# Kernel tuning notes

Measured on AMD Instinct MI355X. Metric: run time of the kernel, lower is better.

Reference implementation:

```python
import jax, jax.numpy as jnp
import numpy as np

N_COARSE, N_FINE, N_EDGE, W, DEPTH = 16384, 65536, 393216, 128, 2


def _mlp_params(key, fan_in, width, out):
    k1, k2 = jax.random.split(key)
    w1 = jax.random.normal(k1, (fan_in, width), jnp.float32) / np.sqrt(fan_in)
    b1 = jnp.zeros((width,), jnp.float32)
    w2 = jax.random.normal(k2, (width, out), jnp.float32) / np.sqrt(width)
    b2 = jnp.zeros((out,), jnp.float32)
    return w1, b1, w2, b2


def setup_inputs() -> dict:
    key = jax.random.key(0)
    ks = jax.random.split(key, 16)
    v = jax.random.normal(ks[0], (N_COARSE, W), jnp.float32)
    c_skip = jax.random.normal(ks[1], (N_FINE, W), jnp.float32)
    e_skip = jax.random.normal(ks[2], (N_EDGE, W), jnp.float32)
    edge_index_skip = jax.random.randint(ks[3], (2, N_EDGE), 0, N_FINE, jnp.int32)
    batch_skip = jnp.zeros((N_FINE,), jnp.int32)  # single graph
    cluster = jax.random.randint(ks[4], (N_FINE,), 0, N_COARSE, jnp.int32)
    rel_pos = jax.random.normal(ks[5], (N_FINE, 1), jnp.float32)  # scalar rel pos (scalar_rel_pos=True)

    # unpooling FNN: (W + 1) -> W -> W
    uw1, ub1, uw2, ub2 = _mlp_params(ks[6], W + 1, W, W)
    # InteractionNetwork MLPs, stacked over DEPTH layers
    ew1 = []; eb1 = []; ew2 = []; eb2 = []
    nw1 = []; nb1 = []; nw2 = []; nb2 = []
    for i in range(DEPTH):
        a, b, c, d = _mlp_params(ks[7 + i], 3 * W, W, W)  # edge MLP: [e, v_s, v_r]
        ew1.append(a); eb1.append(b); ew2.append(c); eb2.append(d)
        a, b, c, d = _mlp_params(ks[9 + i], 2 * W, W, W)  # node MLP: [v, aggr(e)]
        nw1.append(a); nb1.append(b); nw2.append(c); nb2.append(d)
    stk = lambda xs: jnp.stack(xs, 0)
    return {
        'v': v, 'c_skip': c_skip, 'e_skip': e_skip, 'rel_pos': rel_pos,
        'unpool_w1': uw1, 'unpool_b1': ub1, 'unpool_w2': uw2, 'unpool_b2': ub2,
        'edge_w1': stk(ew1), 'edge_b1': stk(eb1), 'edge_w2': stk(ew2), 'edge_b2': stk(eb2),
        'node_w1': stk(nw1), 'node_b1': stk(nb1), 'node_w2': stk(nw2), 'node_b2': stk(nb2),
        'edge_index_skip': edge_index_skip, 'cluster': cluster, 'batch_skip': batch_skip,
    }


def _mlp(x, w1, b1, w2, b2):
    return jax.nn.selu(x @ w1 + b1) @ w2 + b2


def reference(v, c_skip, e_skip, rel_pos,
              unpool_w1, unpool_b1, unpool_w2, unpool_b2,
              edge_w1, edge_b1, edge_w2, edge_b2,
              node_w1, node_b1, node_w2, node_b2,
              edge_index_skip, cluster, batch_skip):
    # --- MeshUpMP: gather coarse features to fine nodes, mix with rel. pos. ---
    h = jnp.concatenate([v[cluster], rel_pos], axis=-1)            # [N_fine, W+1]
    v = _mlp(h, unpool_w1, unpool_b1, unpool_w2, unpool_b2)        # [N_fine, W]
    v = v + c_skip
    e = e_skip
    s, r = edge_index_skip[0], edge_index_skip[1]
    n_nodes = v.shape[0]
    # --- stacked InteractionNetwork layers (residual edge+node updates) ---
    for i in range(edge_w1.shape[0]):
        msg = jnp.concatenate([e, v[s], v[r]], axis=-1)            # [E, 3W]
        e = e + _mlp(msg, edge_w1[i], edge_b1[i], edge_w2[i], edge_b2[i])
        agg = jax.ops.segment_sum(e, r, num_segments=n_nodes)      # sum aggregation
        nin = jnp.concatenate([v, agg], axis=-1)                   # [N, 2W]
        v = v + _mlp(nin, node_w1[i], node_b1[i], node_w2[i], node_b2[i])
    return v
```

## Files before the change

kernel.cpp:

```cpp
#include <hip/hip_runtime.h>
#include <hip/hip_bf16.h>
#include <stdint.h>

#define NCOARSE 16384
#define NFINE   65536
#define NEDGE   393216

typedef __bf16 bf16;
typedef bf16 bf16x8 __attribute__((ext_vector_type(8)));
typedef bf16 bf16x4 __attribute__((ext_vector_type(4)));
typedef float f32x4 __attribute__((ext_vector_type(4)));

__device__ __forceinline__ float selu_f(float x) {
    return x > 0.f ? 1.0507009873554805f * x
                   : 1.7580993408473766f * (__expf(x) - 1.f);
}

__device__ __forceinline__ bf16x8 cvt8(f32x4 lo, f32x4 hi) {
    bf16x8 r;
    r[0] = (bf16)lo[0]; r[1] = (bf16)lo[1]; r[2] = (bf16)lo[2]; r[3] = (bf16)lo[3];
    r[4] = (bf16)hi[0]; r[5] = (bf16)hi[1]; r[6] = (bf16)hi[2]; r[7] = (bf16)hi[3];
    return r;
}

__global__ void prep_weights(const float* __restrict__ uw1, const float* __restrict__ uw2,
                             const float* __restrict__ ew1, const float* __restrict__ ew2,
                             const float* __restrict__ nw1, const float* __restrict__ nw2,
                             bf16* __restrict__ wb)
{
    int i = blockIdx.x * 256 + threadIdx.x;
    float v;
    if (i < 16384) {
        int j = i; int k = (j >> 12) * 32 + (j & 31), n = (j & 4095) >> 5;
        v = uw1[k * 128 + n];
    } else if (i < 32768) {
        int j = i - 16384; int k = (j >> 12) * 32 + (j & 31), n = (j & 4095) >> 5;
        v = uw2[k * 128 + n];
    } else if (i < 131072) {
        int j = i - 32768; int l = j / 49152; j -= l * 49152;
        int k = (j >> 12) * 32 + (j & 31), n = (j & 4095) >> 5;
        v = ew1[l * 49152 + k * 128 + n];
    } else if (i < 163840) {
        int j = i - 131072; int l = j >> 14; j &= 16383;
        int k = (j >> 12) * 32 + (j & 31), n = (j & 4095) >> 5;
        v = ew2[l * 16384 + k * 128 + n];
    } else if (i < 229376) {
        int j = i - 163840; int l = j >> 15; j &= 32767;
        int k = (j >> 12) * 32 + (j & 31), n = (j & 4095) >> 5;
        v = nw1[l * 32768 + k * 128 + n];
    } else {
        int j = i - 229376; int l = j >> 14; j &= 16383;
        int k = (j >> 12) * 32 + (j & 31), n = (j & 4095) >> 5;
        v = nw2[l * 16384 + k * 128 + n];
    }
    wb[i] = (bf16)v;
}

__global__ void hist_kernel(const int* __restrict__ ei, int* __restrict__ cnt) {
    int e = blockIdx.x * 256 + threadIdx.x;
    if (e < NEDGE) atomicAdd(&cnt[ei[NEDGE + e]], 1);
}

__global__ __launch_bounds__(1024)
void scan_kernel(const int* __restrict__ cnt, int* __restrict__ rowptr,
                 int* __restrict__ cursor) {
    __shared__ int part[1024];
    const int t = threadIdx.x;
    const int base = t * 64;
    int s = 0;
    for (int i = 0; i < 64; ++i) s += cnt[base + i];
    part[t] = s;
    __syncthreads();
    for (int off = 1; off < 1024; off <<= 1) {
        int v = (t >= off) ? part[t - off] : 0;
        __syncthreads();
        part[t] += v;
        __syncthreads();
    }
    int run = part[t] - s;
    for (int i = 0; i < 64; ++i) {
        int c = cnt[base + i];
        rowptr[base + i] = run;
        cursor[base + i] = run;
        run += c;
    }
    if (t == 1023) rowptr[65536] = run;
}

__global__ void scatter_kernel(const int* __restrict__ ei, int* __restrict__ cursor,
                               int* __restrict__ perm) {
    int e = blockIdx.x * 256 + threadIdx.x;
    if (e < NEDGE) {
        int r = ei[NEDGE + e];
        int p = atomicAdd(&cursor[r], 1);
        perm[p] = e;
    }
}

__global__ __launch_bounds__(256)
void agg_kernel(const bf16* __restrict__ e, const int* __restrict__ rowptr,
                const int* __restrict__ perm, bf16* __restrict__ agg) {
    int t = blockIdx.x * 256 + threadIdx.x;
    int node = t >> 3, c0 = (t & 7) * 16;
    int s = rowptr[node], en = rowptr[node + 1];
    float acc[16];
    #pragma unroll
    for (int k = 0; k < 16; ++k) acc[k] = 0.f;
    for (int j = s; j < en; ++j) {
        size_t ed = (size_t)perm[j];
        bf16x8 x0 = *(const bf16x8*)(e + ed * 128 + c0);
        bf16x8 x1 = *(const bf16x8*)(e + ed * 128 + c0 + 8);
        #pragma unroll
        for (int k = 0; k < 8; ++k) { acc[k] += (float)x0[k]; acc[8 + k] += (float)x1[k]; }
    }
    bf16x8 o0, o1;
    #pragma unroll
    for (int k = 0; k < 8; ++k) { o0[k] = (bf16)acc[k]; o1[k] = (bf16)acc[8 + k]; }
    *(bf16x8*)(agg + (size_t)node * 128 + c0) = o0;
    *(bf16x8*)(agg + (size_t)node * 128 + c0 + 8) = o1;
}


#define STAGE_LOAD(wp, st0, st1) do { \
    st0 = *(const bf16x8*)((wp) + tid * 8); \
    st1 = *(const bf16x8*)((wp) + 2048 + tid * 8); } while (0)
#define STAGE_WRITE(buf, st0, st1) do { \
    *(bf16x8*)&(buf)[tid >> 2][(tid & 3) * 8] = st0; \
    *(bf16x8*)&(buf)[(tid + 256) >> 2][(tid & 3) * 8] = st1; } while (0)

template<bool EF32>
__global__ __launch_bounds__(256, 2)
void edge_kernel(const void* __restrict__ e_in_v,
                 bf16* __restrict__ e_out,
                 const bf16* __restrict__ v_bf,
                 const int* __restrict__ ei,
                 const bf16* __restrict__ w1s,
                 const float* __restrict__ b1,
                 const bf16* __restrict__ w2s,
                 const float* __restrict__ b2)
{
    const int tid = threadIdx.x;
    const int wv = tid >> 6, lane = tid & 63;
    const int lr = lane & 15, g = lane >> 4;
    const int wbase = blockIdx.x * 128 + wv * 32;

    __shared__ bf16 wl[2][128][40];
    __shared__ bf16 hid_all[4][32][136];
    bf16 (*hid)[136] = hid_all[wv];

    const float* e_f32 = (const float*)e_in_v;
    const bf16*  e_b16 = (const bf16*)e_in_v;

    int row[2], sidx[2], ridx[2];
    #pragma unroll
    for (int mt = 0; mt < 2; ++mt) {
        row[mt] = wbase + mt * 16 + lr;
        sidx[mt] = ei[row[mt]];
        ridx[mt] = ei[NEDGE + row[mt]];
    }

    bf16x8 be[4][2], bs[4][2], br[4][2];
    #pragma unroll
    for (int ks = 0; ks < 4; ++ks)
        #pragma unroll
        for (int mt = 0; mt < 2; ++mt)
            bs[ks][mt] = *(const bf16x8*)(v_bf + (size_t)sidx[mt] * 128 + ks * 32 + g * 8);
    #pragma unroll
    for (int ks = 0; ks < 4; ++ks)
        #pragma unroll
        for (int mt = 0; mt < 2; ++mt)
            br[ks][mt] = *(const bf16x8*)(v_bf + (size_t)ridx[mt] * 128 + ks * 32 + g * 8);
    if (EF32) {
        f32x4 tlo[4][2], thi[4][2];
        #pragma unroll
        for (int ks = 0; ks < 4; ++ks)
            #pragma unroll
            for (int mt = 0; mt < 2; ++mt) {
                const float* p = e_f32 + (size_t)row[mt] * 128 + ks * 32 + g * 8;
                tlo[ks][mt] = *(const f32x4*)p;
                thi[ks][mt] = *(const f32x4*)(p + 4);
            }
        #pragma unroll
        for (int ks = 0; ks < 4; ++ks)
            #pragma unroll
            for (int mt = 0; mt < 2; ++mt)
                be[ks][mt] = cvt8(tlo[ks][mt], thi[ks][mt]);
    } else {
        #pragma unroll
        for (int ks = 0; ks < 4; ++ks)
            #pragma unroll
            for (int mt = 0; mt < 2; ++mt)
                be[ks][mt] = *(const bf16x8*)(e_b16 + (size_t)row[mt] * 128 + ks * 32 + g * 8);
    }

    bf16x8 st0, st1;
    STAGE_LOAD(w1s, st0, st1);
    STAGE_WRITE(wl[0], st0, st1);
    __syncthreads();

    f32x4 acc1[8][2], acc2[8][2];
    #pragma unroll
    for (int oc = 0; oc < 8; ++oc) {
        f32x4 z = {0.f, 0.f, 0.f, 0.f};
        acc1[oc][0] = z; acc1[oc][1] = z;
    }

    f32x4  eof[8][2];
    bf16x4 eob[8][2];

    #pragma unroll
    for (int s = 0; s < 16; ++s) {
        const int cur = s & 1;
        if (s < 15) {
            const bf16* wp = (s + 1 < 12) ? w1s + (size_t)(s + 1) * 4096
                                          : w2s + (size_t)(s + 1 - 12) * 4096;
            STAGE_LOAD(wp, st0, st1);
        }
        if (s == 12) {
            #pragma unroll
            for (int mt = 0; mt < 2; ++mt)
                #pragma unroll
                for (int oc = 0; oc < 8; ++oc) {
                    const int col = oc * 16 + g * 4;
                    if (EF32) eof[oc][mt] = *(const f32x4*)(e_f32 + (size_t)row[mt] * 128 + col);
                    else      eob[oc][mt] = *(const bf16x4*)(e_b16 + (size_t)row[mt] * 128 + col);
                }
        }
        bf16x8 a[8];
        #pragma unroll
        for (int oc = 0; oc < 8; ++oc)
            a[oc] = *(const bf16x8*)&wl[cur][oc * 16 + lr][g * 8];

        if (s < 12) {
            bf16x8 b0 = (s < 4) ? be[s][0] : (s < 8) ? bs[s - 4][0] : br[s - 8][0];
            bf16x8 b1f = (s < 4) ? be[s][1] : (s < 8) ? bs[s - 4][1] : br[s - 8][1];
            #pragma unroll
            for (int oc = 0; oc < 8; ++oc) {
                acc1[oc][0] = __builtin_amdgcn_mfma_f32_16x16x32_bf16(a[oc], b0, acc1[oc][0], 0, 0, 0);
                acc1[oc][1] = __builtin_amdgcn_mfma_f32_16x16x32_bf16(a[oc], b1f, acc1[oc][1], 0, 0, 0);
            }
        } else {
            if (s == 12) {
                #pragma unroll
                for (int oc = 0; oc < 8; ++oc) {
                    f32x4 z = {0.f, 0.f, 0.f, 0.f};
                    acc2[oc][0] = z; acc2[oc][1] = z;
                }
            }
            bf16x8 h0 = *(const bf16x8*)&hid[lr][(s - 12) * 32 + g * 8];
            bf16x8 h1 = *(const bf16x8*)&hid[16 + lr][(s - 12) * 32 + g * 8];
            #pragma unroll
            for (int oc = 0; oc < 8; ++oc) {
                acc2[oc][0] = __builtin_amdgcn_mfma_f32_16x16x32_bf16(a[oc], h0, acc2[oc][0], 0, 0, 0);
                acc2[oc][1] = __builtin_amdgcn_mfma_f32_16x16x32_bf16(a[oc], h1, acc2[oc][1], 0, 0, 0);
            }
        }
        if (s == 11) {
            #pragma unroll
            for (int mt = 0; mt < 2; ++mt)
                #pragma unroll
                for (int oc = 0; oc < 8; ++oc) {
                    const int col = oc * 16 + g * 4;
                    f32x4 bv = *(const f32x4*)(b1 + col);
                    bf16x4 h;
                    #pragma unroll
                    for (int j = 0; j < 4; ++j)
                        h[j] = (bf16)selu_f(acc1[oc][mt][j] + bv[j]);
                    *(bf16x4*)&hid[mt * 16 + lr][col] = h;
                }
        }
        if (s < 15) STAGE_WRITE(wl[cur ^ 1], st0, st1);
        __syncthreads();
    }

    #pragma unroll
    for (int mt = 0; mt < 2; ++mt) {
        const size_t r = row[mt];
        #pragma unroll
        for (int oc = 0; oc < 8; ++oc) {
            const int col = oc * 16 + g * 4;
            f32x4 b2v = *(const f32x4*)(b2 + col);
            bf16x4 stv;
            #pragma unroll
            for (int j = 0; j < 4; ++j) {
                float eo = EF32 ? eof[oc][mt][j] : (float)eob[oc][mt][j];
                stv[j] = (bf16)(eo + acc2[oc][mt][j] + b2v[j]);
            }
            __builtin_nontemporal_store(stv, (bf16x4*)(e_out + r * 128 + col));
        }
    }
}

__global__ __launch_bounds__(256, 2)
void node_kernel(float* __restrict__ v_io,
                 bf16* __restrict__ v_bf,
                 const bf16* __restrict__ agg,
                 const bf16* __restrict__ w1s,
                 const float* __restrict__ b1,
                 const bf16* __restrict__ w2s,
                 const float* __restrict__ b2)
{
    const int tid = threadIdx.x;
    const int wv = tid >> 6, lane = tid & 63;
    const int lr = lane & 15, g = lane >> 4;
    const int wbase = blockIdx.x * 128 + wv * 32;

    __shared__ bf16 wl[2][128][40];
    __shared__ bf16 hid_all[4][32][136];
    bf16 (*hid)[136] = hid_all[wv];

    int row[2];
    row[0] = wbase + lr; row[1] = wbase + 16 + lr;

    bf16x8 bv[4][2], ba[4][2];
    #pragma unroll
    for (int ks = 0; ks < 4; ++ks)
        #pragma unroll
        for (int mt = 0; mt < 2; ++mt)
            bv[ks][mt] = *(const bf16x8*)(v_bf + (size_t)row[mt] * 128 + ks * 32 + g * 8);
    #pragma unroll
    for (int ks = 0; ks < 4; ++ks)
        #pragma unroll
        for (int mt = 0; mt < 2; ++mt)
            ba[ks][mt] = *(const bf16x8*)(agg + (size_t)row[mt] * 128 + ks * 32 + g * 8);

    bf16x8 st0, st1;
    STAGE_LOAD(w1s, st0, st1);
    STAGE_WRITE(wl[0], st0, st1);
    __syncthreads();

    f32x4 acc1[8][2], acc2[8][2], vo[8][2];
    #pragma unroll
    for (int oc = 0; oc < 8; ++oc) {
        f32x4 z = {0.f, 0.f, 0.f, 0.f};
        acc1[oc][0] = z; acc1[oc][1] = z;
    }

    #pragma unroll
    for (int s = 0; s < 12; ++s) {
        const int cur = s & 1;
        if (s < 11) {
            const bf16* wp = (s + 1 < 8) ? w1s + (size_t)(s + 1) * 4096
                                         : w2s + (size_t)(s + 1 - 8) * 4096;
            STAGE_LOAD(wp, st0, st1);
        }
        if (s == 8) {
            #pragma unroll
            for (int mt = 0; mt < 2; ++mt)
                #pragma unroll
                for (int oc = 0; oc < 8; ++oc)
                    vo[oc][mt] = *(const f32x4*)(v_io + (size_t)row[mt] * 128 + oc * 16 + g * 4);
        }
        bf16x8 a[8];
        #pragma unroll
        for (int oc = 0; oc < 8; ++oc)
            a[oc] = *(const bf16x8*)&wl[cur][oc * 16 + lr][g * 8];

        if (s < 8) {
            bf16x8 b0 = (s < 4) ? bv[s][0] : ba[s - 4][0];
            bf16x8 b1f = (s < 4) ? bv[s][1] : ba[s - 4][1];
            #pragma unroll
            for (int oc = 0; oc < 8; ++oc) {
                acc1[oc][0] = __builtin_amdgcn_mfma_f32_16x16x32_bf16(a[oc], b0, acc1[oc][0], 0, 0, 0);
                acc1[oc][1] = __builtin_amdgcn_mfma_f32_16x16x32_bf16(a[oc], b1f, acc1[oc][1], 0, 0, 0);
            }
        } else {
            if (s == 8) {
                #pragma unroll
                for (int oc = 0; oc < 8; ++oc) {
                    f32x4 z = {0.f, 0.f, 0.f, 0.f};
                    acc2[oc][0] = z; acc2[oc][1] = z;
                }
            }
            bf16x8 h0 = *(const bf16x8*)&hid[lr][(s - 8) * 32 + g * 8];
            bf16x8 h1 = *(const bf16x8*)&hid[16 + lr][(s - 8) * 32 + g * 8];
            #pragma unroll
            for (int oc = 0; oc < 8; ++oc) {
                acc2[oc][0] = __builtin_amdgcn_mfma_f32_16x16x32_bf16(a[oc], h0, acc2[oc][0], 0, 0, 0);
                acc2[oc][1] = __builtin_amdgcn_mfma_f32_16x16x32_bf16(a[oc], h1, acc2[oc][1], 0, 0, 0);
            }
        }
        if (s == 7) {
            #pragma unroll
            for (int mt = 0; mt < 2; ++mt)
                #pragma unroll
                for (int oc = 0; oc < 8; ++oc) {
                    const int col = oc * 16 + g * 4;
                    f32x4 bvv = *(const f32x4*)(b1 + col);
                    bf16x4 h;
                    #pragma unroll
                    for (int j = 0; j < 4; ++j)
                        h[j] = (bf16)selu_f(acc1[oc][mt][j] + bvv[j]);
                    *(bf16x4*)&hid[mt * 16 + lr][col] = h;
                }
        }
        if (s < 11) STAGE_WRITE(wl[cur ^ 1], st0, st1);
        __syncthreads();
    }

    #pragma unroll
    for (int mt = 0; mt < 2; ++mt) {
        const size_t r = row[mt];
        #pragma unroll
        for (int oc = 0; oc < 8; ++oc) {
            const int col = oc * 16 + g * 4;
            f32x4 b2v = *(const f32x4*)(b2 + col);
            f32x4 vn; bf16x4 m;
            #pragma unroll
            for (int j = 0; j < 4; ++j) {
                vn[j] = vo[oc][mt][j] + acc2[oc][mt][j] + b2v[j];
                m[j] = (bf16)vn[j];
            }
            *(f32x4*)(v_io + r * 128 + col) = vn;
            *(bf16x4*)(v_bf + r * 128 + col) = m;
        }
    }
}

__global__ __launch_bounds__(256, 2)
void unpool_kernel(const float* __restrict__ v_coarse,
                   const float* __restrict__ c_skip,
                   const float* __restrict__ rel_pos,
                   const float* __restrict__ uw1,
                   const float* __restrict__ b1,
                   const bf16* __restrict__ w1s,
                   const bf16* __restrict__ w2s,
                   const float* __restrict__ b2,
                   const int* __restrict__ cluster,
                   float* __restrict__ v_out,
                   bf16* __restrict__ v_bf)
{
    const int tid = threadIdx.x;
    const int wv = tid >> 6, lane = tid & 63;
    const int lr = lane & 15, g = lane >> 4;
    const int wbase = blockIdx.x * 128 + wv * 32;

    __shared__ bf16 wl[2][128][40];
    __shared__ bf16 hid_all[4][32][136];
    bf16 (*hid)[136] = hid_all[wv];

    int row[2], cl[2]; float relv[2];
    #pragma unroll
    for (int mt = 0; mt < 2; ++mt) {
        row[mt] = wbase + mt * 16 + lr;
        cl[mt] = cluster[row[mt]];
        relv[mt] = rel_pos[row[mt]];
    }

    bf16x8 bfr[4][2];
    {
        f32x4 tlo[4][2], thi[4][2];
        #pragma unroll
        for (int ks = 0; ks < 4; ++ks)
            #pragma unroll
            for (int mt = 0; mt < 2; ++mt) {
                const float* p = v_coarse + (size_t)cl[mt] * 128 + ks * 32 + g * 8;
                tlo[ks][mt] = *(const f32x4*)p;
                thi[ks][mt] = *(const f32x4*)(p + 4);
            }
        #pragma unroll
        for (int ks = 0; ks < 4; ++ks)
            #pragma unroll
            for (int mt = 0; mt < 2; ++mt)
                bfr[ks][mt] = cvt8(tlo[ks][mt], thi[ks][mt]);
    }

    bf16x8 st0, st1;
    STAGE_LOAD(w1s, st0, st1);
    STAGE_WRITE(wl[0], st0, st1);
    __syncthreads();

    f32x4 acc1[8][2], acc2[8][2], cs[8][2];
    #pragma unroll
    for (int oc = 0; oc < 8; ++oc) {
        f32x4 z = {0.f, 0.f, 0.f, 0.f};
        acc1[oc][0] = z; acc1[oc][1] = z;
    }

    #pragma unroll
    for (int s = 0; s < 8; ++s) {
        const int cur = s & 1;
        if (s < 7) {
            const bf16* wp = (s + 1 < 4) ? w1s + (size_t)(s + 1) * 4096
                                         : w2s + (size_t)(s + 1 - 4) * 4096;
            STAGE_LOAD(wp, st0, st1);
        }
        if (s == 4) {
            #pragma unroll
            for (int mt = 0; mt < 2; ++mt)
                #pragma unroll
                for (int oc = 0; oc < 8; ++oc)
                    cs[oc][mt] = *(const f32x4*)(c_skip + (size_t)row[mt] * 128 + oc * 16 + g * 4);
        }
        bf16x8 a[8];
        #pragma unroll
        for (int oc = 0; oc < 8; ++oc)
            a[oc] = *(const bf16x8*)&wl[cur][oc * 16 + lr][g * 8];

        if (s < 4) {
            #pragma unroll
            for (int oc = 0; oc < 8; ++oc) {
                acc1[oc][0] = __builtin_amdgcn_mfma_f32_16x16x32_bf16(a[oc], bfr[s][0], acc1[oc][0], 0, 0, 0);
                acc1[oc][1] = __builtin_amdgcn_mfma_f32_16x16x32_bf16(a[oc], bfr[s][1], acc1[oc][1], 0, 0, 0);
            }
        } else {
            if (s == 4) {
                #pragma unroll
                for (int oc = 0; oc < 8; ++oc) {
                    f32x4 z = {0.f, 0.f, 0.f, 0.f};
                    acc2[oc][0] = z; acc2[oc][1] = z;
                }
            }
            bf16x8 h0 = *(const bf16x8*)&hid[lr][(s - 4) * 32 + g * 8];
            bf16x8 h1 = *(const bf16x8*)&hid[16 + lr][(s - 4) * 32 + g * 8];
            #pragma unroll
            for (int oc = 0; oc < 8; ++oc) {
                acc2[oc][0] = __builtin_amdgcn_mfma_f32_16x16x32_bf16(a[oc], h0, acc2[oc][0], 0, 0, 0);
                acc2[oc][1] = __builtin_amdgcn_mfma_f32_16x16x32_bf16(a[oc], h1, acc2[oc][1], 0, 0, 0);
            }
        }
        if (s == 3) {
            #pragma unroll
            for (int mt = 0; mt < 2; ++mt)
                #pragma unroll
                for (int oc = 0; oc < 8; ++oc) {
                    const int col = oc * 16 + g * 4;
                    f32x4 bvv = *(const f32x4*)(b1 + col);
                    f32x4 wlr = *(const f32x4*)(uw1 + 128 * 128 + col);
                    bf16x4 h;
                    #pragma unroll
                    for (int j = 0; j < 4; ++j)
                        h[j] = (bf16)selu_f(acc1[oc][mt][j] + bvv[j] + relv[mt] * wlr[j]);
                    *(bf16x4*)&hid[mt * 16 + lr][col] = h;
                }
        }
        if (s < 7) STAGE_WRITE(wl[cur ^ 1], st0, st1);
        __syncthreads();
    }

    #pragma unroll
    for (int mt = 0; mt < 2; ++mt) {
        const size_t r = row[mt];
        #pragma unroll
        for (int oc = 0; oc < 8; ++oc) {
            const int col = oc * 16 + g * 4;
            f32x4 b2v = *(const f32x4*)(b2 + col);
            f32x4 vn; bf16x4 m;
            #pragma unroll
            for (int j = 0; j < 4; ++j) {
                vn[j] = acc2[oc][mt][j] + b2v[j] + cs[oc][mt][j];
                m[j] = (bf16)vn[j];
            }
            *(f32x4*)(v_out + r * 128 + col) = vn;
            *(bf16x4*)(v_bf + r * 128 + col) = m;
        }
    }
}

extern "C" void kernel_launch(void* const* d_in, const int* in_sizes, int n_in,
                              void* d_out, int out_size, void* d_ws, size_t ws_size,
                              hipStream_t stream) {
    const float* v_c    = (const float*)d_in[0];
    const float* c_skip = (const float*)d_in[1];
    const float* e_skip = (const float*)d_in[2];
    const float* rel    = (const float*)d_in[3];
    const float* uw1    = (const float*)d_in[4];
    const float* ub1    = (const float*)d_in[5];
    const float* uw2    = (const float*)d_in[6];
    const float* ub2    = (const float*)d_in[7];
    const float* ew1    = (const float*)d_in[8];
    const float* eb1    = (const float*)d_in[9];
    const float* ew2    = (const float*)d_in[10];
    const float* eb2    = (const float*)d_in[11];
    const float* nw1    = (const float*)d_in[12];
    const float* nb1    = (const float*)d_in[13];
    const float* nw2    = (const float*)d_in[14];
    const float* nb2    = (const float*)d_in[15];
    const int*   ei     = (const int*)d_in[16];
    const int*   clus   = (const int*)d_in[17];

    char* ws = (char*)d_ws;
    bf16*  e_bf   = (bf16*)(ws);
    bf16*  v_bf   = (bf16*)(ws + 100663296);
    bf16*  agg    = (bf16*)(ws + 117440512);
    bf16*  wb     = (bf16*)(ws + 134217728);
    int*   cnt    = (int*) (ws + 134742016);
    int*   rowptr = (int*) (ws + 135004160);
    int*   cursor = (int*) (ws + 135266308);
    int*   perm   = (int*) (ws + 135528452);

    float* vout = (float*)d_out;

    prep_weights<<<1024, 256, 0, stream>>>(uw1, uw2, ew1, ew2, nw1, nw2, wb);
    hipMemsetAsync(cnt, 0, 262144, stream);
    hist_kernel<<<1536, 256, 0, stream>>>(ei, cnt);
    scan_kernel<<<1, 1024, 0, stream>>>(cnt, rowptr, cursor);
    scatter_kernel<<<1536, 256, 0, stream>>>(ei, cursor, perm);

    unpool_kernel<<<512, 256, 0, stream>>>(v_c, c_skip, rel, uw1, ub1,
                                           wb + 0, wb + 16384, ub2, clus, vout, v_bf);

    edge_kernel<true><<<3072, 256, 0, stream>>>((const void*)e_skip, e_bf, v_bf, ei,
                                                wb + 32768, eb1, wb + 131072, eb2);
    agg_kernel<<<2048, 256, 0, stream>>>(e_bf, rowptr, perm, agg);
    node_kernel<<<512, 256, 0, stream>>>(vout, v_bf, agg,
                                         wb + 163840, nb1, wb + 229376, nb2);

    edge_kernel<false><<<3072, 256, 0, stream>>>((const void*)e_bf, e_bf, v_bf, ei,
                                                 wb + 32768 + 49152, eb1 + 128,
                                                 wb + 131072 + 16384, eb2 + 128);
    agg_kernel<<<2048, 256, 0, stream>>>(e_bf, rowptr, perm, agg);
    node_kernel<<<512, 256, 0, stream>>>(vout, v_bf, agg,
                                         wb + 163840 + 32768, nb1 + 128, wb + 229376 + 16384, nb2 + 128);
}
```

Before: 553.4 us.

## Precompute per-node sender/receiver projections to shrink edge MLP first layer

Splits the edge MLP's first-layer weight into e, sender and receiver blocks. The sender and receiver products are computed once per node by a new pcalc kernel into a [N,256] buffer P. The edge kernel then gathers the precomputed projections instead of raw node features and runs only the e-part GEMM, which cuts the per-edge first-layer K from 384 to 128. This removes two thirds of the edge layer-1 MFMA work, at the cost of an extra node-level GEMM and gathering 2x128 bf16 projections per edge. Rounding the projections to bf16 before they are summed adds a small numerical difference.

```diff
diff --git a/kernel.cpp b/kernel.cpp
--- a/kernel.cpp
+++ b/kernel.cpp
@@ -48,10 +48,16 @@
         int j = i - 163840; int l = j >> 15; j &= 32767;
         int k = (j >> 12) * 32 + (j & 31), n = (j & 4095) >> 5;
         v = nw1[l * 32768 + k * 128 + n];
-    } else {
+    } else if (i < 262144) {
         int j = i - 229376; int l = j >> 14; j &= 16383;
         int k = (j >> 12) * 32 + (j & 31), n = (j & 4095) >> 5;
         v = nw2[l * 16384 + k * 128 + n];
+    } else {
+        int j = i - 262144; int l = j >> 15; j &= 32767;
+        int seg = j >> 13, n = (j >> 5) & 255, kk = j & 31;
+        int k = seg * 32 + kk;
+        if (n < 128) v = ew1[l * 49152 + (128 + k) * 128 + n];
+        else         v = ew1[l * 49152 + (256 + k) * 128 + (n - 128)];
     }
     wb[i] = (bf16)v;
 }
@@ -120,10 +126,82 @@
     *(bf16x8*)(agg + (size_t)node * 128 + c0 + 8) = o1;
 }
 
-
-#define STAGE_LOAD(wp, st0, st1) do { \
-    st0 = *(const bf16x8*)((wp) + tid * 8); \
-    st1 = *(const bf16x8*)((wp) + 2048 + tid * 8); } while (0)
+__global__ __launch_bounds__(256, 2)
+void pcalc_kernel(const bf16* __restrict__ v_bf,
+                  const bf16* __restrict__ wp,
+                  bf16* __restrict__ P)
+{
+    const int tid = threadIdx.x;
+    const int wv = tid >> 6, lane = tid & 63;
+    const int lr = lane & 15, g = lane >> 4;
+    const int wbase = blockIdx.x * 128 + wv * 32;
+
+    __shared__ bf16 wl[2][256][40];
+
+    int row[2];
+    row[0] = wbase + lr; row[1] = wbase + 16 + lr;
+
+    bf16x8 bv[4][2];
+    #pragma unroll
+    for (int ks = 0; ks < 4; ++ks)
+        #pragma unroll
+        for (int mt = 0; mt < 2; ++mt)
+            bv[ks][mt] = *(const bf16x8*)(v_bf + (size_t)row[mt] * 128 + ks * 32 + g * 8);
+
+    bf16x8 st[4];
+    #pragma unroll
+    for (int c = 0; c < 4; ++c) st[c] = *(const bf16x8*)(wp + c * 2048 + tid * 8);
+    #pragma unroll
+    for (int c = 0; c < 4; ++c)
+        *(bf16x8*)&wl[0][c * 64 + (tid >> 2)][(tid & 3) * 8] = st[c];
+    __syncthreads();
+
+    f32x4 acc[16][2];
+    #pragma unroll
+    for (int oc = 0; oc < 16; ++oc) {
+        f32x4 z = {0.f, 0.f, 0.f, 0.f};
+        acc[oc][0] = z; acc[oc][1] = z;
+    }
+
+    #pragma unroll
+    for (int s = 0; s < 4; ++s) {
+        const int cur = s & 1;
+        if (s < 3) {
+            #pragma unroll
+            for (int c = 0; c < 4; ++c)
+                st[c] = *(const bf16x8*)(wp + (size_t)(s + 1) * 8192 + c * 2048 + tid * 8);
+        }
+        #pragma unroll
+        for (int oc = 0; oc < 16; ++oc) {
+            bf16x8 a = *(const bf16x8*)&wl[cur][oc * 16 + lr][g * 8];
+            acc[oc][0] = __builtin_amdgcn_mfma_f32_16x16x32_bf16(a, bv[s][0], acc[oc][0], 0, 0, 0);
+            acc[oc][1] = __builtin_amdgcn_mfma_f32_16x16x32_bf16(a, bv[s][1], acc[oc][1], 0, 0, 0);
+        }
+        if (s < 3) {
+            #pragma unroll
+            for (int c = 0; c < 4; ++c)
+                *(bf16x8*)&wl[cur ^ 1][c * 64 + (tid >> 2)][(tid & 3) * 8] = st[c];
+        }
+        __syncthreads();
+    }
+
+    #pragma unroll
+    for (int mt = 0; mt < 2; ++mt) {
+        const size_t r = row[mt];
+        #pragma unroll
+        for (int oc = 0; oc < 16; ++oc) {
+            const int col = oc * 16 + g * 4;
+            bf16x4 o;
+            #pragma unroll
+            for (int j = 0; j < 4; ++j) o[j] = (bf16)acc[oc][mt][j];
+            *(bf16x4*)(P + r * 256 + col) = o;
+        }
+    }
+}
+
+#define STAGE_LOAD(wp_, st0, st1) do { \
+    st0 = *(const bf16x8*)((wp_) + tid * 8); \
+    st1 = *(const bf16x8*)((wp_) + 2048 + tid * 8); } while (0)
 #define STAGE_WRITE(buf, st0, st1) do { \
     *(bf16x8*)&(buf)[tid >> 2][(tid & 3) * 8] = st0; \
     *(bf16x8*)&(buf)[(tid + 256) >> 2][(tid & 3) * 8] = st1; } while (0)
@@ -132,9 +210,9 @@
 __global__ __launch_bounds__(256, 2)
 void edge_kernel(const void* __restrict__ e_in_v,
                  bf16* __restrict__ e_out,
-                 const bf16* __restrict__ v_bf,
+                 const bf16* __restrict__ P,
                  const int* __restrict__ ei,
-                 const bf16* __restrict__ w1s,
+                 const bf16* __restrict__ w1e,
                  const float* __restrict__ b1,
                  const bf16* __restrict__ w2s,
                  const float* __restrict__ b2)
@@ -159,17 +237,17 @@
         ridx[mt] = ei[NEDGE + row[mt]];
     }
 
-    bf16x8 be[4][2], bs[4][2], br[4][2];
-    #pragma unroll
-    for (int ks = 0; ks < 4; ++ks)
-        #pragma unroll
-        for (int mt = 0; mt < 2; ++mt)
-            bs[ks][mt] = *(const bf16x8*)(v_bf + (size_t)sidx[mt] * 128 + ks * 32 + g * 8);
-    #pragma unroll
-    for (int ks = 0; ks < 4; ++ks)
-        #pragma unroll
-        for (int mt = 0; mt < 2; ++mt)
-            br[ks][mt] = *(const bf16x8*)(v_bf + (size_t)ridx[mt] * 128 + ks * 32 + g * 8);
+    bf16x4 ps[8][2], pr[8][2];
+    #pragma unroll
+    for (int mt = 0; mt < 2; ++mt)
+        #pragma unroll
+        for (int oc = 0; oc < 8; ++oc) {
+            const int col = oc * 16 + g * 4;
+            ps[oc][mt] = *(const bf16x4*)(P + (size_t)sidx[mt] * 256 + col);
+            pr[oc][mt] = *(const bf16x4*)(P + (size_t)ridx[mt] * 256 + 128 + col);
+        }
+
+    bf16x8 be[4][2];
     if (EF32) {
         f32x4 tlo[4][2], thi[4][2];
         #pragma unroll
@@ -194,7 +272,7 @@
     }
 
     bf16x8 st0, st1;
-    STAGE_LOAD(w1s, st0, st1);
+    STAGE_LOAD(w1e, st0, st1);
     STAGE_WRITE(wl[0], st0, st1);
     __syncthreads();
 
@@ -209,14 +287,14 @@
     bf16x4 eob[8][2];
 
     #pragma unroll
-    for (int s = 0; s < 16; ++s) {
+    for (int s = 0; s < 8; ++s) {
         const int cur = s & 1;
-        if (s < 15) {
-            const bf16* wp = (s + 1 < 12) ? w1s + (size_t)(s + 1) * 4096
-                                          : w2s + (size_t)(s + 1 - 12) * 4096;
-            STAGE_LOAD(wp, st0, st1);
-        }
-        if (s == 12) {
+        if (s < 7) {
+            const bf16* wpn = (s + 1 < 4) ? w1e + (size_t)(s + 1) * 4096
+                                          : w2s + (size_t)(s + 1 - 4) * 4096;
+            STAGE_LOAD(wpn, st0, st1);
+        }
+        if (s == 5) {
             #pragma unroll
             for (int mt = 0; mt < 2; ++mt)
                 #pragma unroll
@@ -231,31 +309,30 @@
         for (int oc = 0; oc < 8; ++oc)
             a[oc] = *(const bf16x8*)&wl[cur][oc * 16 + lr][g * 8];
 
-        if (s < 12) {
-            bf16x8 b0 = (s < 4) ? be[s][0] : (s < 8) ? bs[s - 4][0] : br[s - 8][0];
-            bf16x8 b1f = (s < 4) ? be[s][1] : (s < 8) ? bs[s - 4][1] : br[s - 8][1];
+        if (s < 4) {
             #pragma unroll
             for (int oc = 0; oc < 8; ++oc) {
-                acc1[oc][0] = __builtin_amdgcn_mfma_f32_16x16x32_bf16(a[oc], b0, acc1[oc][0], 0, 0, 0);
-                acc1[oc][1] = __builtin_amdgcn_mfma_f32_16x16x32_bf16(a[oc], b1f, acc1[oc][1], 0, 0, 0);
+                acc1[oc][0] = __builtin_amdgcn_mfma_f32_16x16x32_bf16(a[oc], be[s][0], acc1[oc][0], 0, 0, 0);
+                acc1[oc][1] = __builtin_amdgcn_mfma_f32_16x16x32_bf16(a[oc], be[s][1], acc1[oc][1], 0, 0, 0);
             }
         } else {
-            if (s == 12) {
+            if (s == 4) {
                 #pragma unroll
                 for (int oc = 0; oc < 8; ++oc) {
                     f32x4 z = {0.f, 0.f, 0.f, 0.f};
                     acc2[oc][0] = z; acc2[oc][1] = z;
                 }
             }
-            bf16x8 h0 = *(const bf16x8*)&hid[lr][(s - 12) * 32 + g * 8];
-            bf16x8 h1 = *(const bf16x8*)&hid[16 + lr][(s - 12) * 32 + g * 8];
+            const int k2 = s - 4;
+            bf16x8 h0 = *(const bf16x8*)&hid[lr][k2 * 32 + g * 8];
+            bf16x8 h1 = *(const bf16x8*)&hid[16 + lr][k2 * 32 + g * 8];
             #pragma unroll
             for (int oc = 0; oc < 8; ++oc) {
                 acc2[oc][0] = __builtin_amdgcn_mfma_f32_16x16x32_bf16(a[oc], h0, acc2[oc][0], 0, 0, 0);
                 acc2[oc][1] = __builtin_amdgcn_mfma_f32_16x16x32_bf16(a[oc], h1, acc2[oc][1], 0, 0, 0);
             }
         }
-        if (s == 11) {
+        if (s == 3) {
             #pragma unroll
             for (int mt = 0; mt < 2; ++mt)
                 #pragma unroll
@@ -264,12 +341,15 @@
                     f32x4 bv = *(const f32x4*)(b1 + col);
                     bf16x4 h;
                     #pragma unroll
-                    for (int j = 0; j < 4; ++j)
-                        h[j] = (bf16)selu_f(acc1[oc][mt][j] + bv[j]);
+                    for (int j = 0; j < 4; ++j) {
+                        float x = acc1[oc][mt][j] + bv[j]
+                                + (float)ps[oc][mt][j] + (float)pr[oc][mt][j];
+                        h[j] = (bf16)selu_f(x);
+                    }
                     *(bf16x4*)&hid[mt * 16 + lr][col] = h;
                 }
         }
-        if (s < 15) STAGE_WRITE(wl[cur ^ 1], st0, st1);
+        if (s < 7) STAGE_WRITE(wl[cur ^ 1], st0, st1);
         __syncthreads();
     }
 
@@ -582,16 +662,17 @@
     char* ws = (char*)d_ws;
     bf16*  e_bf   = (bf16*)(ws);
     bf16*  v_bf   = (bf16*)(ws + 100663296);
+    bf16*  Pb     = (bf16*)(ws + 117440512);
     bf16*  agg    = (bf16*)(ws + 117440512);
-    bf16*  wb     = (bf16*)(ws + 134217728);
-    int*   cnt    = (int*) (ws + 134742016);
-    int*   rowptr = (int*) (ws + 135004160);
-    int*   cursor = (int*) (ws + 135266308);
-    int*   perm   = (int*) (ws + 135528452);
+    bf16*  wb     = (bf16*)(ws + 150994944);
+    int*   cnt    = (int*) (ws + 151650304);
+    int*   rowptr = (int*) (ws + 151912448);
+    int*   cursor = (int*) (ws + 152174596);
+    int*   perm   = (int*) (ws + 152436740);
 
     float* vout = (float*)d_out;
 
-    prep_weights<<<1024, 256, 0, stream>>>(uw1, uw2, ew1, ew2, nw1, nw2, wb);
+    prep_weights<<<1280, 256, 0, stream>>>(uw1, uw2, ew1, ew2, nw1, nw2, wb);
     hipMemsetAsync(cnt, 0, 262144, stream);
     hist_kernel<<<1536, 256, 0, stream>>>(ei, cnt);
     scan_kernel<<<1, 1024, 0, stream>>>(cnt, rowptr, cursor);
@@ -600,13 +681,15 @@
     unpool_kernel<<<512, 256, 0, stream>>>(v_c, c_skip, rel, uw1, ub1,
                                            wb + 0, wb + 16384, ub2, clus, vout, v_bf);
 
-    edge_kernel<true><<<3072, 256, 0, stream>>>((const void*)e_skip, e_bf, v_bf, ei,
+    pcalc_kernel<<<512, 256, 0, stream>>>(v_bf, wb + 262144, Pb);
+    edge_kernel<true><<<3072, 256, 0, stream>>>((const void*)e_skip, e_bf, Pb, ei,
                                                 wb + 32768, eb1, wb + 131072, eb2);
     agg_kernel<<<2048, 256, 0, stream>>>(e_bf, rowptr, perm, agg);
     node_kernel<<<512, 256, 0, stream>>>(vout, v_bf, agg,
                                          wb + 163840, nb1, wb + 229376, nb2);
 
-    edge_kernel<false><<<3072, 256, 0, stream>>>((const void*)e_bf, e_bf, v_bf, ei,
+    pcalc_kernel<<<512, 256, 0, stream>>>(v_bf, wb + 262144 + 32768, Pb);
+    edge_kernel<false><<<3072, 256, 0, stream>>>((const void*)e_bf, e_bf, Pb, ei,
                                                  wb + 32768 + 49152, eb1 + 128,
                                                  wb + 131072 + 16384, eb2 + 128);
     agg_kernel<<<2048, 256, 0, stream>>>(e_bf, rowptr, perm, agg);
```

Measured after the change: 558.3 us. About the same (+0.9%).
